# Kernel optimization log

Hardware: AMD Instinct MI355X
Metric: run time of the kernel (lower is better)

The kernel has to match this reference:

```python
import jax, jax.numpy as jnp
import numpy as np

UP_RATIO = 2
DOWN_RATIO = 2
K = 12  # hard-coded filter size assumed by the fused kernel


def kaiser_sinc_filter1d(cutoff, half_width, kernel_size):
    # Exact replica of BigVGAN's kaiser_sinc_filter1d (even kernel branch).
    half_size = kernel_size // 2
    delta_f = 4.0 * half_width
    A = 2.285 * (half_size - 1) * np.pi * delta_f + 7.95
    if A > 50.0:
        beta = 0.1102 * (A - 8.7)
    elif A >= 21.0:
        beta = 0.5842 * (A - 21.0) ** 0.4 + 0.07886 * (A - 21.0)
    else:
        beta = 0.0
    window = np.kaiser(kernel_size, beta)  # symmetric, == torch.kaiser_window(periodic=False)
    time = np.arange(-half_size, half_size) + 0.5  # even kernel size
    filt = 2.0 * cutoff * window * np.sinc(2.0 * cutoff * time)
    filt = filt / filt.sum()
    return filt.astype(np.float32)


def setup_inputs() -> dict:
    key = jax.random.key(0)
    k1, k2, k3 = jax.random.split(key, 3)
    B, C, T = 16, 512, 8192
    x = jax.random.normal(k1, (B, C, T), dtype=jnp.float32)
    # log-scale SnakeBeta parameters (alpha_logscale=True -> params stored in log space)
    alpha = jax.random.normal(k2, (C,), dtype=jnp.float32) * 0.1
    beta = jax.random.normal(k3, (C,), dtype=jnp.float32) * 0.1
    up_filter = jnp.asarray(kaiser_sinc_filter1d(0.5 / UP_RATIO, 0.6 / UP_RATIO, K))
    down_filter = jnp.asarray(kaiser_sinc_filter1d(0.5 / DOWN_RATIO, 0.6 / DOWN_RATIO, K))
    return {"x": x, "up_filter": up_filter, "down_filter": down_filter,
            "alpha": alpha, "beta": beta}


def _depthwise_conv(x, filt, stride=1, lhs_dilation=1, pad=(0, 0)):
    # x: (B, C, T); shared 1-tap-bank depthwise conv: fold channels into batch.
    B, C, T = x.shape
    xr = x.reshape(B * C, 1, T)
    w = filt.reshape(1, 1, -1)
    out = jax.lax.conv_general_dilated(
        xr, w, window_strides=(stride,), padding=[pad],
        lhs_dilation=(lhs_dilation,),
        dimension_numbers=("NCH", "OIH", "NCH"))
    return out.reshape(B, C, -1)


def reference(x, up_filter, down_filter, alpha, beta):
    B, C, T = x.shape
    # ---- UpSample1d(ratio=2, kernel_size=12): replicate pad + conv_transpose ----
    pad = K // UP_RATIO - 1                              # 5
    pad_left = pad * UP_RATIO + (K - UP_RATIO) // 2      # 15
    pad_right = pad * UP_RATIO + (K - UP_RATIO + 1) // 2  # 15
    xp = jnp.pad(x, ((0, 0), (0, 0), (pad, pad)), mode="edge")
    # conv_transpose1d(stride=s) == lhs-dilated conv with flipped kernel, full padding
    up = UP_RATIO * _depthwise_conv(xp, up_filter[::-1],
                                    lhs_dilation=UP_RATIO, pad=(K - 1, K - 1))
    up = up[..., pad_left: up.shape[-1] - pad_right]      # (B, C, 2T)
    # ---- SnakeBeta activation (log-scale alpha/beta) ----
    a = jnp.exp(alpha)[None, :, None]
    b = jnp.exp(beta)[None, :, None]
    act = up + (1.0 / (b + 1e-9)) * jnp.sin(up * a) ** 2
    # ---- DownSample1d: replicate-padded lowpass FIR, stride 2 ----
    dl = K // 2 - 1   # 5 (even kernel)
    dr = K // 2       # 6
    actp = jnp.pad(act, ((0, 0), (0, 0), (dl, dr)), mode="edge")
    out = _depthwise_conv(actp, down_filter, stride=DOWN_RATIO)  # (B, C, T)
    return out
```

## Files before the change

kernel.cpp:

```cpp
#include <hip/hip_runtime.h>


#define T_LEN 8192
#define C_CH  512
#define B_N   16
#define W     8
#define BLOCK 256

typedef float f2 __attribute__((ext_vector_type(2)));
typedef float f4 __attribute__((ext_vector_type(4)));

__device__ __forceinline__ f2 pk_mul(f2 a, f2 b) {
    f2 d; asm("v_pk_mul_f32 %0, %1, %2" : "=v"(d) : "v"(a), "v"(b)); return d;
}
__device__ __forceinline__ f2 pk_mul_bx(f2 a, f2 b) {
    f2 d; asm("v_pk_mul_f32 %0, %1, %2 op_sel:[0,0] op_sel_hi:[1,0]" : "=v"(d) : "v"(a), "v"(b)); return d;
}
__device__ __forceinline__ f2 pk_mul_by(f2 a, f2 b) {
    f2 d; asm("v_pk_mul_f32 %0, %1, %2 op_sel:[0,1] op_sel_hi:[1,1]" : "=v"(d) : "v"(a), "v"(b)); return d;
}
__device__ __forceinline__ void pk_fma(f2& acc, f2 a, f2 b) {
    asm("v_pk_fma_f32 %0, %1, %2, %0" : "+v"(acc) : "v"(a), "v"(b));
}
__device__ __forceinline__ void pk_fma_bx(f2& acc, f2 a, f2 b) {
    asm("v_pk_fma_f32 %0, %1, %2, %0 op_sel:[0,0,0] op_sel_hi:[1,0,1]" : "+v"(acc) : "v"(a), "v"(b));
}
__device__ __forceinline__ void pk_fma_by(f2& acc, f2 a, f2 b) {
    asm("v_pk_fma_f32 %0, %1, %2, %0 op_sel:[0,1,0] op_sel_hi:[1,1,1]" : "+v"(acc) : "v"(a), "v"(b));
}
__device__ __forceinline__ float hw_sin(float x_rev) {
    float r; asm("v_sin_f32 %0, %1" : "=v"(r) : "v"(x_rev)); return r;
}

__global__ __launch_bounds__(BLOCK) void act1d_kernel(
    const float* __restrict__ x,
    const float* __restrict__ uf_g,
    const float* __restrict__ df_g,
    const float* __restrict__ alpha,
    const float* __restrict__ beta,
    float* __restrict__ out)
{
    const int T = T_LEN;
    const int bid = blockIdx.x;
    const int row = bid >> 2;
    const int chunk = bid & 3;
    const int c = row & (C_CH - 1);
    const int nb = chunk * (BLOCK * W) + (int)threadIdx.x * W;
    const long rowoff = (long)row * T;
    const float* xrow = x + rowoff;

    f2 ufp[6], dfp[6];
    const f2* ufv = (const f2*)uf_g;
    const f2* dfv = (const f2*)df_g;
#pragma unroll
    for (int m = 0; m < 6; ++m) {
        f2 u = ufv[m];
        ufp[m].x = 2.0f * u.x; ufp[m].y = 2.0f * u.y;
        dfp[m] = dfv[m];
    }

    const float ea_r = __expf(alpha[c]) * 0.15915494309189535f;
    const float invb = 1.0f / (__expf(beta[c]) + 1e-9f);
    f2 eap; eap.x = ea_r; eap.y = ea_r;
    f2 ibp; ibp.x = invb; ibp.y = invb;

    f2 a2[13];

    const bool interior = (nb >= 8) && (nb + 16 <= T);
    if (interior) {
        f2 xx[12];
        const f4* xv4 = (const f4*)(xrow + nb - 8);
#pragma unroll
        for (int k = 0; k < 6; ++k) {
            f4 v = xv4[k];
            xx[2*k].x   = v.x; xx[2*k].y   = v.y;
            xx[2*k+1].x = v.z; xx[2*k+1].y = v.w;
        }
#pragma unroll
        for (int p = 0; p < 13; ++p) {
            f2 u;
            {
                const int w = p + 8;
                if (w & 1) u = pk_mul_by(ufp[0], xx[w >> 1]);
                else       u = pk_mul_bx(ufp[0], xx[w >> 1]);
            }
#pragma unroll
            for (int m = 1; m < 6; ++m) {
                const int w = p + 8 - m;
                if (w & 1) pk_fma_by(u, ufp[m], xx[w >> 1]);
                else       pk_fma_bx(u, ufp[m], xx[w >> 1]);
            }
            f2 s = pk_mul(u, eap);
            f2 sv; sv.x = hw_sin(s.x); sv.y = hw_sin(s.y);
            f2 t = pk_mul(sv, ibp);
            f2 av = u;
            pk_fma(av, t, sv);
            a2[p] = av;
        }
    } else {
#pragma unroll
        for (int j = 0; j < 26; ++j) {
            int t = 2*nb - 5 + j;
            t = min(max(t, 0), 2*T - 1);
            const int s = t >> 1;
            const int par = t & 1;
            float xv7[7];
#pragma unroll
            for (int m = 0; m < 7; ++m) {
                int g = s - 3 + m;
                g = min(max(g, 0), T - 1);
                xv7[m] = xrow[g];
            }
            const float upo = ufp[0].x*xv7[6] + ufp[1].x*xv7[5] + ufp[2].x*xv7[4]
                            + ufp[3].x*xv7[3] + ufp[4].x*xv7[2] + ufp[5].x*xv7[1];
            const float upe = ufp[0].y*xv7[5] + ufp[1].y*xv7[4] + ufp[2].y*xv7[3]
                            + ufp[3].y*xv7[2] + ufp[4].y*xv7[1] + ufp[5].y*xv7[0];
            const float up = par ? upo : upe;
            const float sv = hw_sin(up * ea_r);
            const float aj = fmaf(invb * sv, sv, up);
            if (j & 1) a2[j >> 1].y = aj; else a2[j >> 1].x = aj;
        }
    }

    float o[W];
#pragma unroll
    for (int d = 0; d < W; ++d) {
        f2 acc = pk_mul(dfp[0], a2[d]);
#pragma unroll
        for (int m = 1; m < 6; ++m) pk_fma(acc, dfp[m], a2[d + m]);
        o[d] = acc.x + acc.y;
    }
    f4* ov = (f4*)(out + rowoff + nb);
    f4 o0; o0.x = o[0]; o0.y = o[1]; o0.z = o[2]; o0.w = o[3];
    f4 o1; o1.x = o[4]; o1.y = o[5]; o1.z = o[6]; o1.w = o[7];
    __builtin_nontemporal_store(o0, ov);
    __builtin_nontemporal_store(o1, ov + 1);
}

extern "C" void kernel_launch(void* const* d_in, const int* in_sizes, int n_in,
                              void* d_out, int out_size, void* d_ws, size_t ws_size,
                              hipStream_t stream) {
    const float* x  = (const float*)d_in[0];
    const float* uf = (const float*)d_in[1];
    const float* df = (const float*)d_in[2];
    const float* al = (const float*)d_in[3];
    const float* be = (const float*)d_in[4];
    float* outp = (float*)d_out;

    const int grid = B_N * C_CH * (T_LEN / (BLOCK * W));
    act1d_kernel<<<grid, BLOCK, 0, stream>>>(x, uf, df, al, be, outp);
}
```

Measured before the change: 463.7 us.

## Process whole row per block with register double-buffered input prefetch

Each block now handles a full row of the sequence over four iterations instead of one quarter-row chunk, and the grid shrinks fourfold. Input for the next iteration is loaded into a second register buffer while the current one is computed, which is meant to hide global-load latency and amortise the per-block setup (filter and alpha/beta loads, exp). Nontemporal stores become plain stores. The cost is higher register pressure from the double buffer, which may lower occupancy, and fewer blocks in flight.

```diff
diff --git a/kernel.cpp b/kernel.cpp
--- a/kernel.cpp
+++ b/kernel.cpp
@@ -6,6 +6,7 @@
 #define B_N   16
 #define W     8
 #define BLOCK 256
+#define ITERS 4
 
 typedef float f2 __attribute__((ext_vector_type(2)));
 typedef float f4 __attribute__((ext_vector_type(4)));
@@ -41,13 +42,12 @@
     float* __restrict__ out)
 {
     const int T = T_LEN;
-    const int bid = blockIdx.x;
-    const int row = bid >> 2;
-    const int chunk = bid & 3;
+    const int row = blockIdx.x;
     const int c = row & (C_CH - 1);
-    const int nb = chunk * (BLOCK * W) + (int)threadIdx.x * W;
     const long rowoff = (long)row * T;
     const float* xrow = x + rowoff;
+    float* orow = out + rowoff;
+    const int t0 = (int)threadIdx.x * W;
 
     f2 ufp[6], dfp[6];
     const f2* ufv = (const f2*)uf_g;
@@ -64,77 +64,102 @@
     f2 eap; eap.x = ea_r; eap.y = ea_r;
     f2 ibp; ibp.x = invb; ibp.y = invb;
 
-    f2 a2[13];
+    f2 xb[2][12];
 
-    const bool interior = (nb >= 8) && (nb + 16 <= T);
-    if (interior) {
-        f2 xx[12];
-        const f4* xv4 = (const f4*)(xrow + nb - 8);
+    {
+        const int nb = t0;
+        const float* lb = xrow + min(max(nb - 8, 0), T - 24);
+        const f4* p4 = (const f4*)lb;
 #pragma unroll
         for (int k = 0; k < 6; ++k) {
-            f4 v = xv4[k];
-            xx[2*k].x   = v.x; xx[2*k].y   = v.y;
-            xx[2*k+1].x = v.z; xx[2*k+1].y = v.w;
-        }
-#pragma unroll
-        for (int p = 0; p < 13; ++p) {
-            f2 u;
-            {
-                const int w = p + 8;
-                if (w & 1) u = pk_mul_by(ufp[0], xx[w >> 1]);
-                else       u = pk_mul_bx(ufp[0], xx[w >> 1]);
-            }
-#pragma unroll
-            for (int m = 1; m < 6; ++m) {
-                const int w = p + 8 - m;
-                if (w & 1) pk_fma_by(u, ufp[m], xx[w >> 1]);
-                else       pk_fma_bx(u, ufp[m], xx[w >> 1]);
-            }
-            f2 s = pk_mul(u, eap);
-            f2 sv; sv.x = hw_sin(s.x); sv.y = hw_sin(s.y);
-            f2 t = pk_mul(sv, ibp);
-            f2 av = u;
-            pk_fma(av, t, sv);
-            a2[p] = av;
-        }
-    } else {
-#pragma unroll
-        for (int j = 0; j < 26; ++j) {
-            int t = 2*nb - 5 + j;
-            t = min(max(t, 0), 2*T - 1);
-            const int s = t >> 1;
-            const int par = t & 1;
-            float xv7[7];
-#pragma unroll
-            for (int m = 0; m < 7; ++m) {
-                int g = s - 3 + m;
-                g = min(max(g, 0), T - 1);
-                xv7[m] = xrow[g];
-            }
-            const float upo = ufp[0].x*xv7[6] + ufp[1].x*xv7[5] + ufp[2].x*xv7[4]
-                            + ufp[3].x*xv7[3] + ufp[4].x*xv7[2] + ufp[5].x*xv7[1];
-            const float upe = ufp[0].y*xv7[5] + ufp[1].y*xv7[4] + ufp[2].y*xv7[3]
-                            + ufp[3].y*xv7[2] + ufp[4].y*xv7[1] + ufp[5].y*xv7[0];
-            const float up = par ? upo : upe;
-            const float sv = hw_sin(up * ea_r);
-            const float aj = fmaf(invb * sv, sv, up);
-            if (j & 1) a2[j >> 1].y = aj; else a2[j >> 1].x = aj;
+            f4 v = p4[k];
+            xb[0][2*k].x   = v.x; xb[0][2*k].y   = v.y;
+            xb[0][2*k+1].x = v.z; xb[0][2*k+1].y = v.w;
         }
     }
 
-    float o[W];
 #pragma unroll
-    for (int d = 0; d < W; ++d) {
-        f2 acc = pk_mul(dfp[0], a2[d]);
+    for (int it = 0; it < ITERS; ++it) {
+        const int cur = it & 1;
+        const int nxt = cur ^ 1;
+        const int nb = it * (BLOCK * W) + t0;
+
+        if (it + 1 < ITERS) {
+            const int nb2 = (it + 1) * (BLOCK * W) + t0;
+            const float* lb = xrow + min(max(nb2 - 8, 0), T - 24);
+            const f4* p4 = (const f4*)lb;
 #pragma unroll
-        for (int m = 1; m < 6; ++m) pk_fma(acc, dfp[m], a2[d + m]);
-        o[d] = acc.x + acc.y;
+            for (int k = 0; k < 6; ++k) {
+                f4 v = p4[k];
+                xb[nxt][2*k].x   = v.x; xb[nxt][2*k].y   = v.y;
+                xb[nxt][2*k+1].x = v.z; xb[nxt][2*k+1].y = v.w;
+            }
+        }
+
+        f2 a2[13];
+
+        const bool interior = (it > 0 && it < ITERS - 1) || ((nb >= 8) && (nb + 16 <= T));
+        if (interior) {
+#pragma unroll
+            for (int p = 0; p < 13; ++p) {
+                f2 u;
+                {
+                    const int w = p + 8;
+                    if (w & 1) u = pk_mul_by(ufp[0], xb[cur][w >> 1]);
+                    else       u = pk_mul_bx(ufp[0], xb[cur][w >> 1]);
+                }
+#pragma unroll
+                for (int m = 1; m < 6; ++m) {
+                    const int w = p + 8 - m;
+                    if (w & 1) pk_fma_by(u, ufp[m], xb[cur][w >> 1]);
+                    else       pk_fma_bx(u, ufp[m], xb[cur][w >> 1]);
+                }
+                f2 s = pk_mul(u, eap);
+                f2 sv; sv.x = hw_sin(s.x); sv.y = hw_sin(s.y);
+                f2 tt = pk_mul(sv, ibp);
+                f2 av = u;
+                pk_fma(av, tt, sv);
+                a2[p] = av;
+            }
+        } else {
+#pragma unroll
+            for (int j = 0; j < 26; ++j) {
+                int t = 2*nb - 5 + j;
+                t = min(max(t, 0), 2*T - 1);
+                const int s = t >> 1;
+                const int par = t & 1;
+                float xv7[7];
+#pragma unroll
+                for (int m = 0; m < 7; ++m) {
+                    int g = s - 3 + m;
+                    g = min(max(g, 0), T - 1);
+                    xv7[m] = xrow[g];
+                }
+                const float upo = ufp[0].x*xv7[6] + ufp[1].x*xv7[5] + ufp[2].x*xv7[4]
+                                + ufp[3].x*xv7[3] + ufp[4].x*xv7[2] + ufp[5].x*xv7[1];
+                const float upe = ufp[0].y*xv7[5] + ufp[1].y*xv7[4] + ufp[2].y*xv7[3]
+                                + ufp[3].y*xv7[2] + ufp[4].y*xv7[1] + ufp[5].y*xv7[0];
+                const float up = par ? upo : upe;
+                const float sv = hw_sin(up * ea_r);
+                const float aj = fmaf(invb * sv, sv, up);
+                if (j & 1) a2[j >> 1].y = aj; else a2[j >> 1].x = aj;
+            }
+        }
+
+        float o[W];
+#pragma unroll
+        for (int d = 0; d < W; ++d) {
+            f2 acc = pk_mul(dfp[0], a2[d]);
+#pragma unroll
+            for (int m = 1; m < 6; ++m) pk_fma(acc, dfp[m], a2[d + m]);
+            o[d] = acc.x + acc.y;
+        }
+        f4* ov = (f4*)(orow + nb);
+        f4 o0; o0.x = o[0]; o0.y = o[1]; o0.z = o[2]; o0.w = o[3];
+        f4 o1; o1.x = o[4]; o1.y = o[5]; o1.z = o[6]; o1.w = o[7];
+        ov[0] = o0;
+        ov[1] = o1;
     }
-    f4* ov = (f4*)(out + rowoff + nb);
-    f4 o0; o0.x = o[0]; o0.y = o[1]; o0.z = o[2]; o0.w = o[3];
-    f4 o1; o1.x = o[4]; o1.y = o[5]; o1.z = o[6]; o1.w = o[7];
-    __builtin_nontemporal_store(o0, ov);
-    __builtin_nontemporal_store(o1, ov + 1);
 }
 
 extern "C" void kernel_launch(void* const* d_in, const int* in_sizes, int n_in,
@@ -147,6 +172,6 @@
     const float* be = (const float*)d_in[4];
     float* outp = (float*)d_out;
 
-    const int grid = B_N * C_CH * (T_LEN / (BLOCK * W));
+    const int grid = B_N * C_CH;
     act1d_kernel<<<grid, BLOCK, 0, stream>>>(x, uf, df, al, be, outp);
 }
```

New measurement: 443.7 us. 4.3% less time.
